# Kernel tuning notes

Measured on AMD Instinct MI355X. Metric: run time of the kernel, lower is better.

The kernel has to match this reference:

```python
import jax, jax.numpy as jnp
import numpy as np

K1 = 20
K2 = 6
LAMBDA = 0.3
MARGIN = 0.03


def _pairwise_sq(x, y):
    # squared euclidean distance (standard re-ID pairwise_distance, clamped at 0)
    xx = jnp.sum(x * x, axis=1)
    yy = jnp.sum(y * y, axis=1)
    d = xx[:, None] + yy[None, :] - 2.0 * (x @ y.T)
    return jnp.maximum(d, 0.0)


def _recip_mask(R, k):
    # boolean (N,N) mask: M[i,j]=True iff j is in i's top-(k+1) AND i is in j's top-(k+1)
    N = R.shape[0]
    topk = R[:, : k + 1]                       # (N, k+1)
    back = topk[topk]                          # (N, k+1, k+1)
    cond = jnp.any(back == jnp.arange(N)[:, None, None], axis=2)  # (N, k+1)
    rows = jnp.broadcast_to(jnp.arange(N)[:, None], topk.shape)
    return jnp.zeros((N, N), bool).at[rows, topk].set(cond)


def _rerank_dist(feat):
    n = feat.shape[0]
    feats = jnp.concatenate([feat, feat], axis=0)      # feat1 == feat2 == inputs
    N = feats.shape[0]
    D = _pairwise_sq(feats, feats)                     # (N, N)
    original = D.T                                     # original_dist (symmetric)
    # eval_type=True: gallery columns replaced by global max before ranking
    maxv = D.max()
    dist = jnp.concatenate([D[:, :n], jnp.full((N, N - n), maxv, D.dtype)], axis=1)
    R = jnp.argsort(dist, axis=1)                      # stable argsort
    K = _recip_mask(R, K1)                             # k-reciprocal sets
    Khalf = _recip_mask(R, int(round(K1 / 2)))         # half-size reciprocal sets
    Kf = K.astype(jnp.float32)
    Khf = Khalf.astype(jnp.float32)
    inter = Kf @ Khf.T                                 # inter[i,j] = |Khalf[j] & K[i]|
    sizes = Khf.sum(axis=1)                            # |Khalf[j]|
    expand = K & (inter > (2.0 / 3.0) * sizes[None, :])
    E = K | ((expand.astype(jnp.float32) @ Khf) > 0)   # expanded reciprocal sets
    W = jnp.exp(-original) * E
    s = W.sum(axis=1, keepdims=True)
    V = W / jnp.where(s == 0, 1.0, s)                  # rows with empty sets stay zero
    # local query expansion over top-k2 neighbors
    V = V[R[:, :K2]].mean(axis=1)                      # (N, N)

    def jrow(vi):
        # sum_j min(V[i,j], V[t,j]) over all t; zeros contribute nothing (matches invIndex)
        tmin = jnp.sum(jnp.minimum(vi[None, :], V), axis=1)   # (N,)
        return 1.0 - tmin / (2.0 - tmin)

    jac = jax.lax.map(jax.checkpoint(jrow), V[:n])     # (n, N)
    final = jac * (1.0 - LAMBDA) + original[:n] * LAMBDA
    return final[:, n:]                                # (n, n)


def setup_inputs() -> dict:
    key = jax.random.key(0)
    k1, k2 = jax.random.split(key)
    x = jax.random.normal(k1, (1024, 2048), jnp.float32)
    x = x / jnp.linalg.norm(x, axis=1, keepdims=True)  # L2-normalized re-ID embeddings
    targets = jax.random.randint(k2, (1024,), 0, 128)
    return {"inputs": x, "targets": targets}


def reference(inputs, targets):
    dist = _rerank_dist(inputs)                        # (n, n)
    mask = targets[:, None] == targets[None, :]
    dist_ap = jnp.where(mask, dist, -jnp.inf).max(axis=1)
    dist_an = jnp.where(mask, jnp.inf, dist).min(axis=1)
    # MarginRankingLoss(dist_an, dist_ap, y=1) = mean(relu(dist_ap - dist_an + margin))
    loss = jnp.mean(jax.nn.relu(dist_ap - dist_an + MARGIN))
    return (loss, dist, dist_ap, dist_an)
```

## Files before the change

kernel.cpp:

```cpp
#include <hip/hip_runtime.h>

#define N 1024
#define DIM 2048

typedef unsigned long long u64;

__device__ __forceinline__ u64 umin64(u64 a, u64 b){ return a < b ? a : b; }

__device__ __forceinline__ void tri_map(int lid, int* by, int* bx){
  int y = (int)((sqrtf(8.0f * lid + 1.0f) - 1.0f) * 0.5f);
  while ((y + 1) * (y + 2) / 2 <= lid) y++;
  while (y * (y + 1) / 2 > lid) y--;
  *by = y;
  *bx = lid - y * (y + 1) / 2;
}

__global__ __launch_bounds__(256) void rownorm_kernel(const float* __restrict__ x, float* __restrict__ xx){
  int i = blockIdx.x, t = threadIdx.x;
  const float4* row = (const float4*)(x + (size_t)i * DIM);
  float s = 0.f;
  #pragma unroll
  for (int q = 0; q < 2; q++){
    float4 v = row[t + q*256];
    s += v.x*v.x + v.y*v.y + v.z*v.z + v.w*v.w;
  }
  #pragma unroll
  for (int off = 32; off > 0; off >>= 1) s += __shfl_down(s, off);
  __shared__ float sm[4];
  if ((t & 63) == 0) sm[t >> 6] = s;
  __syncthreads();
  if (t == 0) xx[i] = sm[0] + sm[1] + sm[2] + sm[3];
}

__global__ __launch_bounds__(256) void gemm_split_kernel(const float* __restrict__ x,
    float* __restrict__ p0, float* __restrict__ p1, int kc){
  __shared__ __align__(16) float As[32][64];
  __shared__ __align__(16) float Bs[32][64];
  int by, bx; tri_map(blockIdx.x, &by, &bx);
  int z = blockIdx.y;
  int t = threadIdx.x;
  int tx = t & 15, ty = t >> 4;
  int i0 = by * 64, j0 = bx * 64;
  int kbase = z * kc;
  float acc[4][4] = {};
  for (int k0 = kbase; k0 < kbase + kc; k0 += 32){
    #pragma unroll
    for (int e = 0; e < 2; e++){
      int idx = t + e*256;
      int row = idx >> 3, kq = idx & 7;
      float4 fa = *(const float4*)&x[(size_t)(i0+row)*DIM + k0 + kq*4];
      float4 fb = *(const float4*)&x[(size_t)(j0+row)*DIM + k0 + kq*4];
      int sw = kq << 3;
      float va[4] = {fa.x, fa.y, fa.z, fa.w};
      float vb[4] = {fb.x, fb.y, fb.z, fb.w};
      #pragma unroll
      for (int e2 = 0; e2 < 4; e2++){
        As[kq*4+e2][row ^ sw] = va[e2];
        Bs[kq*4+e2][row ^ sw] = vb[e2];
      }
    }
    __syncthreads();
    #pragma unroll
    for (int kk = 0; kk < 32; kk++){
      int sw = (kk >> 2) << 3;
      float4 a4 = *(const float4*)&As[kk][(ty*4) ^ sw];
      float4 b4 = *(const float4*)&Bs[kk][(tx*4) ^ sw];
      float av[4] = {a4.x, a4.y, a4.z, a4.w};
      float bv[4] = {b4.x, b4.y, b4.z, b4.w};
      #pragma unroll
      for (int r = 0; r < 4; r++){
        #pragma unroll
        for (int c = 0; c < 4; c++) acc[r][c] = fmaf(av[r], bv[c], acc[r][c]);
      }
    }
    __syncthreads();
  }
  float* P = (z == 0) ? p0 : p1 + (size_t)(z - 1) * N * N;
  #pragma unroll
  for (int r = 0; r < 4; r++){
    #pragma unroll
    for (int c = 0; c < 4; c++){
      int i = i0 + ty*4 + r, j = j0 + tx*4 + c;
      P[(size_t)i * N + j] = acc[r][c];
    }
  }
}

__global__ __launch_bounds__(256) void gemm_combine_kernel(
    const float* __restrict__ p0, const float* __restrict__ p1,
    int nsplit, const float* __restrict__ xx, float* __restrict__ D){
  __shared__ float Ts[64][68];
  int by, bx; tri_map(blockIdx.x, &by, &bx);
  int t = threadIdx.x;
  int tc = t & 15, tr = t >> 4;
  int i0 = by * 64, j0 = bx * 64;
  float4 xj = *(const float4*)&xx[j0 + tc*4];
  #pragma unroll
  for (int rr = 0; rr < 4; rr++){
    int i = i0 + tr*4 + rr;
    size_t off = (size_t)i * N + j0 + tc*4;
    float4 s = *(const float4*)&p0[off];
    for (int z = 1; z < nsplit; z++){
      float4 q = *(const float4*)&p1[(size_t)(z-1)*N*N + off];
      s.x += q.x; s.y += q.y; s.z += q.z; s.w += q.w;
    }
    float xxi = xx[i];
    float4 o;
    o.x = xxi + xj.x - 2.0f*s.x; o.x = (o.x > 0.f) ? o.x : 0.f;
    o.y = xxi + xj.y - 2.0f*s.y; o.y = (o.y > 0.f) ? o.y : 0.f;
    o.z = xxi + xj.z - 2.0f*s.z; o.z = (o.z > 0.f) ? o.z : 0.f;
    o.w = xxi + xj.w - 2.0f*s.w; o.w = (o.w > 0.f) ? o.w : 0.f;
    *(float4*)&D[off] = o;
    Ts[tr*4+rr][tc*4+0] = o.x; Ts[tr*4+rr][tc*4+1] = o.y;
    Ts[tr*4+rr][tc*4+2] = o.z; Ts[tr*4+rr][tc*4+3] = o.w;
  }
  if (by == bx) return;
  __syncthreads();
  #pragma unroll
  for (int rr = 0; rr < 4; rr++){
    int jrow = j0 + tr*4 + rr;
    float4 o;
    o.x = Ts[tc*4+0][tr*4+rr];
    o.y = Ts[tc*4+1][tr*4+rr];
    o.z = Ts[tc*4+2][tr*4+rr];
    o.w = Ts[tc*4+3][tr*4+rr];
    *(float4*)&D[(size_t)jrow * N + i0 + tc*4] = o;
  }
}

__global__ __launch_bounds__(64) void topk_kernel(const float* __restrict__ D, int* __restrict__ T){
  int i = blockIdx.x, t = threadIdx.x;
  const float* row = D + (size_t)i * N;
  u64 key[16];
  #pragma unroll
  for (int q = 0; q < 4; q++){
    int l0 = t*4 + q*256;
    float4 f = *(const float4*)&row[l0];
    key[q*4+0] = ((u64)__float_as_uint(f.x) << 32) | (unsigned)(l0+0);
    key[q*4+1] = ((u64)__float_as_uint(f.y) << 32) | (unsigned)(l0+1);
    key[q*4+2] = ((u64)__float_as_uint(f.z) << 32) | (unsigned)(l0+2);
    key[q*4+3] = ((u64)__float_as_uint(f.w) << 32) | (unsigned)(l0+3);
  }
  for (int it = 0; it < 21; ++it){
    u64 m = key[0];
    #pragma unroll
    for (int q = 1; q < 16; q++) m = umin64(m, key[q]);
    #pragma unroll
    for (int off = 1; off < 64; off <<= 1) m = umin64(m, __shfl_xor(m, off));
    if (t == 0) T[i*21 + it] = (int)(m & 0xffffffffull);
    #pragma unroll
    for (int q = 0; q < 16; q++) if (key[q] == m) key[q] = ~0ull;
  }
}

__global__ __launch_bounds__(64) void recip_kernel(const int* __restrict__ T,
                                                   u64* __restrict__ Kb, u64* __restrict__ Khb){
  int i = blockIdx.x, t = threadIdx.x;
  __shared__ u64 kb[16], khb[16];
  if (t < 16){ kb[t] = 0; khb[t] = 0; }
  __syncthreads();
  if (t < 21){
    int j = T[i*21 + t];
    bool r21 = false, r11 = false;
    for (int p = 0; p < 21; p++){
      if (T[j*21 + p] == i){ r21 = true; if (p < 11) r11 = true; }
    }
    if (r21) atomicOr(&kb[j >> 6], 1ull << (j & 63));
    if (t < 11 && r11) atomicOr(&khb[j >> 6], 1ull << (j & 63));
  }
  __syncthreads();
  if (t < 16){ Kb[i*16 + t] = kb[t]; Khb[i*16 + t] = khb[t]; }
}

__global__ __launch_bounds__(64) void expand_kernel(const u64* __restrict__ Kb,
                                                    const u64* __restrict__ Khb,
                                                    u64* __restrict__ Eb){
  int i = blockIdx.x;
  int lane = threadIdx.x;
  __shared__ u64 er[16];
  __shared__ int js[32];
  __shared__ int njs;
  if (lane == 0) njs = 0;
  __syncthreads();
  if (lane < 16){
    u64 w = Kb[i*16 + lane];
    er[lane] = w;
    while (w){
      int bit = __ffsll((long long)w) - 1;
      w &= w - 1;
      int pos = atomicAdd(&njs, 1);
      js[pos] = lane*64 + bit;
    }
  }
  __syncthreads();
  if (lane < njs){
    int j = js[lane];
    int inter = 0, sz = 0;
    #pragma unroll
    for (int w = 0; w < 16; w++){
      u64 kh = Khb[(size_t)j*16 + w];
      u64 kw = Kb[(size_t)i*16 + w];
      inter += __popcll(kw & kh);
      sz += __popcll(kh);
    }
    if (3*inter > 2*sz){
      #pragma unroll
      for (int w = 0; w < 16; w++){
        u64 kh = Khb[(size_t)j*16 + w];
        if (kh) atomicOr(&er[w], kh);
      }
    }
  }
  __syncthreads();
  if (lane < 16) Eb[i*16 + lane] = er[lane];
}

__global__ __launch_bounds__(256) void v_kernel(const float* __restrict__ Dm,
                                                const u64* __restrict__ Eb,
                                                float* __restrict__ V){
  int i = blockIdx.x, t = threadIdx.x;
  float w[4];
  #pragma unroll
  for (int q = 0; q < 4; q++){
    int l = t + q*256;
    u64 word = Eb[i*16 + (l >> 6)];
    float e = expf(-Dm[(size_t)i * N + l]);
    w[q] = ((word >> (l & 63)) & 1ull) ? e : 0.f;
  }
  float s = w[0] + w[1] + w[2] + w[3];
  #pragma unroll
  for (int off = 32; off > 0; off >>= 1) s += __shfl_down(s, off);
  __shared__ float sm[4];
  __shared__ float stot;
  if ((t & 63) == 0) sm[t >> 6] = s;
  __syncthreads();
  if (t == 0){ float S = sm[0] + sm[1] + sm[2] + sm[3]; stot = (S == 0.f) ? 1.f : S; }
  __syncthreads();
  float denom = stot;
  #pragma unroll
  for (int q = 0; q < 4; q++){
    int l = t + q*256;
    V[(size_t)i * N + l] = w[q] / denom;
  }
}

__global__ __launch_bounds__(256) void vbar_kernel(const float* __restrict__ V,
                                                   const int* __restrict__ T,
                                                   float* __restrict__ Vb){
  int i = blockIdx.x, t = threadIdx.x;
  int t6[6];
  #pragma unroll
  for (int p = 0; p < 6; p++) t6[p] = T[i*21 + p];
  #pragma unroll
  for (int q = 0; q < 4; q++){
    int l = t + q*256;
    float s = 0.f;
    #pragma unroll
    for (int p = 0; p < 6; p++) s += V[(size_t)t6[p] * N + l];
    Vb[(size_t)i * N + l] = s / 6.0f;
  }
}

__global__ __launch_bounds__(256) void jac_split_kernel(const float* __restrict__ Vb,
    float* __restrict__ p0, float* __restrict__ p1, int kc){
  __shared__ __align__(16) float As[32][64];
  __shared__ __align__(16) float Bs[32][64];
  int by, bx; tri_map(blockIdx.x, &by, &bx);
  int z = blockIdx.y;
  int t = threadIdx.x;
  int tx = t & 15, ty = t >> 4;
  int i0 = by * 64, j0 = bx * 64;
  int kbase = z * kc;
  float acc[4][4] = {};
  for (int k0 = kbase; k0 < kbase + kc; k0 += 32){
    #pragma unroll
    for (int e = 0; e < 2; e++){
      int idx = t + e*256;
      int row = idx >> 3, kq = idx & 7;
      float4 fa = *(const float4*)&Vb[(size_t)(i0+row)*N + k0 + kq*4];
      float4 fb = *(const float4*)&Vb[(size_t)(j0+row)*N + k0 + kq*4];
      int sw = kq << 3;
      float va[4] = {fa.x, fa.y, fa.z, fa.w};
      float vb[4] = {fb.x, fb.y, fb.z, fb.w};
      #pragma unroll
      for (int e2 = 0; e2 < 4; e2++){
        As[kq*4+e2][row ^ sw] = va[e2];
        Bs[kq*4+e2][row ^ sw] = vb[e2];
      }
    }
    __syncthreads();
    #pragma unroll
    for (int kk = 0; kk < 32; kk++){
      int sw = (kk >> 2) << 3;
      float4 a4 = *(const float4*)&As[kk][(ty*4) ^ sw];
      float4 b4 = *(const float4*)&Bs[kk][(tx*4) ^ sw];
      float av[4] = {a4.x, a4.y, a4.z, a4.w};
      float bv[4] = {b4.x, b4.y, b4.z, b4.w};
      #pragma unroll
      for (int r = 0; r < 4; r++){
        #pragma unroll
        for (int c = 0; c < 4; c++) acc[r][c] += fminf(av[r], bv[c]);
      }
    }
    __syncthreads();
  }
  float* P = (z == 0) ? p0 : p1 + (size_t)(z - 1) * N * N;
  #pragma unroll
  for (int r = 0; r < 4; r++){
    #pragma unroll
    for (int c = 0; c < 4; c++){
      int i = i0 + ty*4 + r, j = j0 + tx*4 + c;
      P[(size_t)i * N + j] = acc[r][c];
    }
  }
}

__global__ __launch_bounds__(256) void jac_combine_kernel(
    const float* __restrict__ p0, const float* __restrict__ p1,
    int nsplit, float* __restrict__ Dm){
  __shared__ float Ts[64][68];
  int by, bx; tri_map(blockIdx.x, &by, &bx);
  int t = threadIdx.x;
  int tc = t & 15, tr = t >> 4;
  int i0 = by * 64, j0 = bx * 64;
  #pragma unroll
  for (int rr = 0; rr < 4; rr++){
    int i = i0 + tr*4 + rr;
    size_t off = (size_t)i * N + j0 + tc*4;
    float4 s = *(const float4*)&p0[off];
    for (int z = 1; z < nsplit; z++){
      float4 q = *(const float4*)&p1[(size_t)(z-1)*N*N + off];
      s.x += q.x; s.y += q.y; s.z += q.z; s.w += q.w;
    }
    float4 d0 = *(const float4*)&Dm[off];
    float4 o;
    o.x = 0.7f * (1.0f - s.x / (2.0f - s.x)) + 0.3f * d0.x;
    o.y = 0.7f * (1.0f - s.y / (2.0f - s.y)) + 0.3f * d0.y;
    o.z = 0.7f * (1.0f - s.z / (2.0f - s.z)) + 0.3f * d0.z;
    o.w = 0.7f * (1.0f - s.w / (2.0f - s.w)) + 0.3f * d0.w;
    *(float4*)&Dm[off] = o;
    Ts[tr*4+rr][tc*4+0] = o.x; Ts[tr*4+rr][tc*4+1] = o.y;
    Ts[tr*4+rr][tc*4+2] = o.z; Ts[tr*4+rr][tc*4+3] = o.w;
  }
  if (by == bx) return;
  __syncthreads();
  #pragma unroll
  for (int rr = 0; rr < 4; rr++){
    int jrow = j0 + tr*4 + rr;
    float4 o;
    o.x = Ts[tc*4+0][tr*4+rr];
    o.y = Ts[tc*4+1][tr*4+rr];
    o.z = Ts[tc*4+2][tr*4+rr];
    o.w = Ts[tc*4+3][tr*4+rr];
    *(float4*)&Dm[(size_t)jrow * N + i0 + tc*4] = o;
  }
}

__global__ __launch_bounds__(256) void apan_kernel(const float* __restrict__ Dm,
                                                   const int* __restrict__ tg,
                                                   float* __restrict__ ap, float* __restrict__ an){
  int i = blockIdx.x, t = threadIdx.x;
  int ti = tg[i];
  float mx = -3.402823466e38f, mn = 3.402823466e38f;
  #pragma unroll
  for (int q = 0; q < 4; q++){
    int l = t + q*256;
    float v = Dm[(size_t)i * N + l];
    if (tg[l] == ti) mx = fmaxf(mx, v); else mn = fminf(mn, v);
  }
  #pragma unroll
  for (int off = 32; off > 0; off >>= 1){
    mx = fmaxf(mx, __shfl_down(mx, off));
    mn = fminf(mn, __shfl_down(mn, off));
  }
  __shared__ float smx[4], smn[4];
  if ((t & 63) == 0){ smx[t >> 6] = mx; smn[t >> 6] = mn; }
  __syncthreads();
  if (t == 0){
    ap[i] = fmaxf(fmaxf(smx[0], smx[1]), fmaxf(smx[2], smx[3]));
    an[i] = fminf(fminf(smn[0], smn[1]), fminf(smn[2], smn[3]));
  }
}

__global__ __launch_bounds__(256) void loss_kernel(const float* __restrict__ ap,
                                                   const float* __restrict__ an,
                                                   float* __restrict__ out){
  int t = threadIdx.x;
  float s = 0.f;
  #pragma unroll
  for (int q = 0; q < 4; q++){
    int l = t + q*256;
    s += fmaxf(ap[l] - an[l] + 0.03f, 0.f);
  }
  #pragma unroll
  for (int off = 32; off > 0; off >>= 1) s += __shfl_down(s, off);
  __shared__ float sm[4];
  if ((t & 63) == 0) sm[t >> 6] = s;
  __syncthreads();
  if (t == 0) out[0] = (sm[0] + sm[1] + sm[2] + sm[3]) / 1024.0f;
}

static const size_t XX_OFF  = 0;
static const size_t T_OFF   = 4096;
static const size_t KB_OFF  = 90112;
static const size_t KHB_OFF = 221184;
static const size_t EB_OFF  = 352256;
static const size_t V_OFF   = 483328;
static const size_t VB_OFF  = 4677632;
static const size_t P1_OFF  = 8871936;
static const size_t NN4     = 4194304;

extern "C" void kernel_launch(void* const* d_in, const int* in_sizes, int n_in,
                              void* d_out, int out_size, void* d_ws, size_t ws_size,
                              hipStream_t stream){
  const float* x  = (const float*)d_in[0];
  const int*   tg = (const int*)d_in[1];
  float* out = (float*)d_out;
  char* ws = (char*)d_ws;
  if (ws_size < P1_OFF) return;

  float* xx  = (float*)(ws + XX_OFF);
  int*   T   = (int*)(ws + T_OFF);
  u64*   Kb  = (u64*)(ws + KB_OFF);
  u64*   Khb = (u64*)(ws + KHB_OFF);
  u64*   Eb  = (u64*)(ws + EB_OFF);
  float* V   = (float*)(ws + V_OFF);
  float* Vb  = (float*)(ws + VB_OFF);

  float* dist = out + 1;
  float* ap   = out + 1 + (size_t)N*N;
  float* an   = ap + N;

  size_t avail = ws_size - P1_OFF;
  int nsplit = (avail >= 7*NN4) ? 8 : (avail >= 3*NN4) ? 4 : (avail >= 1*NN4) ? 2 : 1;
  float* P0 = V;
  float* P1 = (float*)(ws + P1_OFF);

  rownorm_kernel     <<<N, 256, 0, stream>>>(x, xx);
  gemm_split_kernel  <<<dim3(136, nsplit), 256, 0, stream>>>(x, P0, P1, DIM/nsplit);
  gemm_combine_kernel<<<136, 256, 0, stream>>>(P0, P1, nsplit, xx, dist);
  topk_kernel        <<<N, 64, 0, stream>>>(dist, T);
  recip_kernel       <<<N, 64, 0, stream>>>(T, Kb, Khb);
  expand_kernel      <<<N, 64, 0, stream>>>(Kb, Khb, Eb);
  v_kernel           <<<N, 256, 0, stream>>>(dist, Eb, V);
  vbar_kernel        <<<N, 256, 0, stream>>>(V, T, Vb);
  jac_split_kernel   <<<dim3(136, nsplit), 256, 0, stream>>>(Vb, P0, P1, N/nsplit);
  jac_combine_kernel <<<136, 256, 0, stream>>>(P0, P1, nsplit, dist);
  apan_kernel        <<<N, 256, 0, stream>>>(dist, tg, ap, an);
  loss_kernel        <<<1, 256, 0, stream>>>(ap, an, out);
}
```

Before: 155.5 us.

## Register-prefetch next K slab in split GEMMs and halve combine tiles

The two split-K GEMM-like kernels now load the next 32-wide K slab into registers right after the barrier, so global loads overlap the inner FMA/min loop instead of stalling before it. The combine kernels now launch twice as many blocks, each handling 32 rows of a 64x64 tile with a smaller transpose buffer, to give the partial-sum reduction more parallelism. The cost is extra registers for the prefetched float4s and more, smaller blocks in the combine step.

```diff
diff --git a/kernel.cpp b/kernel.cpp
--- a/kernel.cpp
+++ b/kernel.cpp
@@ -42,29 +42,43 @@
   int tx = t & 15, ty = t >> 4;
   int i0 = by * 64, j0 = bx * 64;
   int kbase = z * kc;
+  int nslab = kc >> 5;
+  int row0 = t >> 3, kq = t & 7;
+  int sw = kq << 3;
+
+  float4 fa0 = *(const float4*)&x[(size_t)(i0+row0)*DIM    + kbase + kq*4];
+  float4 fa1 = *(const float4*)&x[(size_t)(i0+row0+32)*DIM + kbase + kq*4];
+  float4 fb0 = *(const float4*)&x[(size_t)(j0+row0)*DIM    + kbase + kq*4];
+  float4 fb1 = *(const float4*)&x[(size_t)(j0+row0+32)*DIM + kbase + kq*4];
+
   float acc[4][4] = {};
-  for (int k0 = kbase; k0 < kbase + kc; k0 += 32){
-    #pragma unroll
-    for (int e = 0; e < 2; e++){
-      int idx = t + e*256;
-      int row = idx >> 3, kq = idx & 7;
-      float4 fa = *(const float4*)&x[(size_t)(i0+row)*DIM + k0 + kq*4];
-      float4 fb = *(const float4*)&x[(size_t)(j0+row)*DIM + k0 + kq*4];
-      int sw = kq << 3;
-      float va[4] = {fa.x, fa.y, fa.z, fa.w};
-      float vb[4] = {fb.x, fb.y, fb.z, fb.w};
+  for (int s = 0; s < nslab; s++){
+    {
+      float va0[4] = {fa0.x, fa0.y, fa0.z, fa0.w};
+      float va1[4] = {fa1.x, fa1.y, fa1.z, fa1.w};
+      float vb0[4] = {fb0.x, fb0.y, fb0.z, fb0.w};
+      float vb1[4] = {fb1.x, fb1.y, fb1.z, fb1.w};
       #pragma unroll
       for (int e2 = 0; e2 < 4; e2++){
-        As[kq*4+e2][row ^ sw] = va[e2];
-        Bs[kq*4+e2][row ^ sw] = vb[e2];
+        As[kq*4+e2][row0 ^ sw]      = va0[e2];
+        As[kq*4+e2][(row0+32) ^ sw] = va1[e2];
+        Bs[kq*4+e2][row0 ^ sw]      = vb0[e2];
+        Bs[kq*4+e2][(row0+32) ^ sw] = vb1[e2];
       }
     }
     __syncthreads();
+    if (s + 1 < nslab){
+      int k0 = kbase + (s+1)*32;
+      fa0 = *(const float4*)&x[(size_t)(i0+row0)*DIM    + k0 + kq*4];
+      fa1 = *(const float4*)&x[(size_t)(i0+row0+32)*DIM + k0 + kq*4];
+      fb0 = *(const float4*)&x[(size_t)(j0+row0)*DIM    + k0 + kq*4];
+      fb1 = *(const float4*)&x[(size_t)(j0+row0+32)*DIM + k0 + kq*4];
+    }
     #pragma unroll
     for (int kk = 0; kk < 32; kk++){
-      int sw = (kk >> 2) << 3;
-      float4 a4 = *(const float4*)&As[kk][(ty*4) ^ sw];
-      float4 b4 = *(const float4*)&Bs[kk][(tx*4) ^ sw];
+      int swk = (kk >> 2) << 3;
+      float4 a4 = *(const float4*)&As[kk][(ty*4) ^ swk];
+      float4 b4 = *(const float4*)&Bs[kk][(tx*4) ^ swk];
       float av[4] = {a4.x, a4.y, a4.z, a4.w};
       float bv[4] = {b4.x, b4.y, b4.z, b4.w};
       #pragma unroll
@@ -89,15 +103,17 @@
 __global__ __launch_bounds__(256) void gemm_combine_kernel(
     const float* __restrict__ p0, const float* __restrict__ p1,
     int nsplit, const float* __restrict__ xx, float* __restrict__ D){
-  __shared__ float Ts[64][68];
+  __shared__ float Ts[32][68];
   int by, bx; tri_map(blockIdx.x, &by, &bx);
+  int h = blockIdx.y;
   int t = threadIdx.x;
   int tc = t & 15, tr = t >> 4;
-  int i0 = by * 64, j0 = bx * 64;
+  int i0 = by * 64 + h * 32, j0 = bx * 64;
   float4 xj = *(const float4*)&xx[j0 + tc*4];
   #pragma unroll
-  for (int rr = 0; rr < 4; rr++){
-    int i = i0 + tr*4 + rr;
+  for (int rr = 0; rr < 2; rr++){
+    int r = tr*2 + rr;
+    int i = i0 + r;
     size_t off = (size_t)i * N + j0 + tc*4;
     float4 s = *(const float4*)&p0[off];
     for (int z = 1; z < nsplit; z++){
@@ -111,20 +127,21 @@
     o.z = xxi + xj.z - 2.0f*s.z; o.z = (o.z > 0.f) ? o.z : 0.f;
     o.w = xxi + xj.w - 2.0f*s.w; o.w = (o.w > 0.f) ? o.w : 0.f;
     *(float4*)&D[off] = o;
-    Ts[tr*4+rr][tc*4+0] = o.x; Ts[tr*4+rr][tc*4+1] = o.y;
-    Ts[tr*4+rr][tc*4+2] = o.z; Ts[tr*4+rr][tc*4+3] = o.w;
+    Ts[r][tc*4+0] = o.x; Ts[r][tc*4+1] = o.y;
+    Ts[r][tc*4+2] = o.z; Ts[r][tc*4+3] = o.w;
   }
   if (by == bx) return;
   __syncthreads();
-  #pragma unroll
-  for (int rr = 0; rr < 4; rr++){
-    int jrow = j0 + tr*4 + rr;
+  int tc2 = t & 7, jr0 = t >> 3;
+  #pragma unroll
+  for (int e = 0; e < 2; e++){
+    int c = jr0 + e*32;
     float4 o;
-    o.x = Ts[tc*4+0][tr*4+rr];
-    o.y = Ts[tc*4+1][tr*4+rr];
-    o.z = Ts[tc*4+2][tr*4+rr];
-    o.w = Ts[tc*4+3][tr*4+rr];
-    *(float4*)&D[(size_t)jrow * N + i0 + tc*4] = o;
+    o.x = Ts[tc2*4+0][c];
+    o.y = Ts[tc2*4+1][c];
+    o.z = Ts[tc2*4+2][c];
+    o.w = Ts[tc2*4+3][c];
+    *(float4*)&D[(size_t)(j0 + c) * N + i0 + tc2*4] = o;
   }
 }
 
@@ -271,29 +288,43 @@
   int tx = t & 15, ty = t >> 4;
   int i0 = by * 64, j0 = bx * 64;
   int kbase = z * kc;
+  int nslab = kc >> 5;
+  int row0 = t >> 3, kq = t & 7;
+  int sw = kq << 3;
+
+  float4 fa0 = *(const float4*)&Vb[(size_t)(i0+row0)*N    + kbase + kq*4];
+  float4 fa1 = *(const float4*)&Vb[(size_t)(i0+row0+32)*N + kbase + kq*4];
+  float4 fb0 = *(const float4*)&Vb[(size_t)(j0+row0)*N    + kbase + kq*4];
+  float4 fb1 = *(const float4*)&Vb[(size_t)(j0+row0+32)*N + kbase + kq*4];
+
   float acc[4][4] = {};
-  for (int k0 = kbase; k0 < kbase + kc; k0 += 32){
-    #pragma unroll
-    for (int e = 0; e < 2; e++){
-      int idx = t + e*256;
-      int row = idx >> 3, kq = idx & 7;
-      float4 fa = *(const float4*)&Vb[(size_t)(i0+row)*N + k0 + kq*4];
-      float4 fb = *(const float4*)&Vb[(size_t)(j0+row)*N + k0 + kq*4];
-      int sw = kq << 3;
-      float va[4] = {fa.x, fa.y, fa.z, fa.w};
-      float vb[4] = {fb.x, fb.y, fb.z, fb.w};
+  for (int s = 0; s < nslab; s++){
+    {
+      float va0[4] = {fa0.x, fa0.y, fa0.z, fa0.w};
+      float va1[4] = {fa1.x, fa1.y, fa1.z, fa1.w};
+      float vb0[4] = {fb0.x, fb0.y, fb0.z, fb0.w};
+      float vb1[4] = {fb1.x, fb1.y, fb1.z, fb1.w};
       #pragma unroll
       for (int e2 = 0; e2 < 4; e2++){
-        As[kq*4+e2][row ^ sw] = va[e2];
-        Bs[kq*4+e2][row ^ sw] = vb[e2];
+        As[kq*4+e2][row0 ^ sw]      = va0[e2];
+        As[kq*4+e2][(row0+32) ^ sw] = va1[e2];
+        Bs[kq*4+e2][row0 ^ sw]      = vb0[e2];
+        Bs[kq*4+e2][(row0+32) ^ sw] = vb1[e2];
       }
     }
     __syncthreads();
+    if (s + 1 < nslab){
+      int k0 = kbase + (s+1)*32;
+      fa0 = *(const float4*)&Vb[(size_t)(i0+row0)*N    + k0 + kq*4];
+      fa1 = *(const float4*)&Vb[(size_t)(i0+row0+32)*N + k0 + kq*4];
+      fb0 = *(const float4*)&Vb[(size_t)(j0+row0)*N    + k0 + kq*4];
+      fb1 = *(const float4*)&Vb[(size_t)(j0+row0+32)*N + k0 + kq*4];
+    }
     #pragma unroll
     for (int kk = 0; kk < 32; kk++){
-      int sw = (kk >> 2) << 3;
-      float4 a4 = *(const float4*)&As[kk][(ty*4) ^ sw];
-      float4 b4 = *(const float4*)&Bs[kk][(tx*4) ^ sw];
+      int swk = (kk >> 2) << 3;
+      float4 a4 = *(const float4*)&As[kk][(ty*4) ^ swk];
+      float4 b4 = *(const float4*)&Bs[kk][(tx*4) ^ swk];
       float av[4] = {a4.x, a4.y, a4.z, a4.w};
       float bv[4] = {b4.x, b4.y, b4.z, b4.w};
       #pragma unroll
@@ -318,14 +349,16 @@
 __global__ __launch_bounds__(256) void jac_combine_kernel(
     const float* __restrict__ p0, const float* __restrict__ p1,
     int nsplit, float* __restrict__ Dm){
-  __shared__ float Ts[64][68];
+  __shared__ float Ts[32][68];
   int by, bx; tri_map(blockIdx.x, &by, &bx);
+  int h = blockIdx.y;
   int t = threadIdx.x;
   int tc = t & 15, tr = t >> 4;
-  int i0 = by * 64, j0 = bx * 64;
-  #pragma unroll
-  for (int rr = 0; rr < 4; rr++){
-    int i = i0 + tr*4 + rr;
+  int i0 = by * 64 + h * 32, j0 = bx * 64;
+  #pragma unroll
+  for (int rr = 0; rr < 2; rr++){
+    int r = tr*2 + rr;
+    int i = i0 + r;
     size_t off = (size_t)i * N + j0 + tc*4;
     float4 s = *(const float4*)&p0[off];
     for (int z = 1; z < nsplit; z++){
@@ -339,20 +372,21 @@
     o.z = 0.7f * (1.0f - s.z / (2.0f - s.z)) + 0.3f * d0.z;
     o.w = 0.7f * (1.0f - s.w / (2.0f - s.w)) + 0.3f * d0.w;
     *(float4*)&Dm[off] = o;
-    Ts[tr*4+rr][tc*4+0] = o.x; Ts[tr*4+rr][tc*4+1] = o.y;
-    Ts[tr*4+rr][tc*4+2] = o.z; Ts[tr*4+rr][tc*4+3] = o.w;
+    Ts[r][tc*4+0] = o.x; Ts[r][tc*4+1] = o.y;
+    Ts[r][tc*4+2] = o.z; Ts[r][tc*4+3] = o.w;
   }
   if (by == bx) return;
   __syncthreads();
-  #pragma unroll
-  for (int rr = 0; rr < 4; rr++){
-    int jrow = j0 + tr*4 + rr;
+  int tc2 = t & 7, jr0 = t >> 3;
+  #pragma unroll
+  for (int e = 0; e < 2; e++){
+    int c = jr0 + e*32;
     float4 o;
-    o.x = Ts[tc*4+0][tr*4+rr];
-    o.y = Ts[tc*4+1][tr*4+rr];
-    o.z = Ts[tc*4+2][tr*4+rr];
-    o.w = Ts[tc*4+3][tr*4+rr];
-    *(float4*)&Dm[(size_t)jrow * N + i0 + tc*4] = o;
+    o.x = Ts[tc2*4+0][c];
+    o.y = Ts[tc2*4+1][c];
+    o.z = Ts[tc2*4+2][c];
+    o.w = Ts[tc2*4+3][c];
+    *(float4*)&Dm[(size_t)(j0 + c) * N + i0 + tc2*4] = o;
   }
 }
 
@@ -438,14 +472,14 @@
 
   rownorm_kernel     <<<N, 256, 0, stream>>>(x, xx);
   gemm_split_kernel  <<<dim3(136, nsplit), 256, 0, stream>>>(x, P0, P1, DIM/nsplit);
-  gemm_combine_kernel<<<136, 256, 0, stream>>>(P0, P1, nsplit, xx, dist);
+  gemm_combine_kernel<<<dim3(136, 2), 256, 0, stream>>>(P0, P1, nsplit, xx, dist);
   topk_kernel        <<<N, 64, 0, stream>>>(dist, T);
   recip_kernel       <<<N, 64, 0, stream>>>(T, Kb, Khb);
   expand_kernel      <<<N, 64, 0, stream>>>(Kb, Khb, Eb);
   v_kernel           <<<N, 256, 0, stream>>>(dist, Eb, V);
   vbar_kernel        <<<N, 256, 0, stream>>>(V, T, Vb);
   jac_split_kernel   <<<dim3(136, nsplit), 256, 0, stream>>>(Vb, P0, P1, N/nsplit);
-  jac_combine_kernel <<<136, 256, 0, stream>>>(P0, P1, nsplit, dist);
+  jac_combine_kernel <<<dim3(136, 2), 256, 0, stream>>>(P0, P1, nsplit, dist);
   apan_kernel        <<<N, 256, 0, stream>>>(dist, tg, ap, an);
   loss_kernel        <<<1, 256, 0, stream>>>(ap, an, out);
 }
```

Result: faster. 144.3 us, median of 2 (-7.2%).
